# Kernel optimization log

Hardware: AMD Instinct MI355X
Metric: run time of the kernel (lower is better)

The kernel has to match this reference:

```python
import jax, jax.numpy as jnp
import numpy as np

HID = 512       # hidden_dim (embed/LSTM input)
HDE = 512       # hidden_dim_de == attn_channels (required by conv_att channel count)
NCLS = 7000
LSEQ = 40
B = 128
FH, FW = 8, 32


def setup_inputs() -> dict:
    key = jax.random.key(0)
    ks = jax.random.split(key, 16)
    s = 0.05
    inp = {
        "hidden_en": jax.random.normal(ks[0], (1, B, HID), jnp.float32),
        "x_em": jax.random.normal(ks[1], (B, HDE, FH, FW), jnp.float32),
        "att_x_em": jax.random.normal(ks[2], (B, FH * FW, HDE), jnp.float32),
        "target": jax.random.randint(ks[3], (B, LSEQ), 0, NCLS),
        "feature_h": FH,
        "feature_w": FW,
        # parameters
        "embed_w": jax.random.normal(ks[4], (NCLS, HID), jnp.float32) * s,
        "W_ih": jax.random.normal(ks[5], (4 * HDE, HID), jnp.float32) * s,   # LSTMCell input weights (i,f,g,o)
        "W_hh": jax.random.normal(ks[6], (4 * HDE, HDE), jnp.float32) * s,
        "b_ih": jax.random.normal(ks[7], (4 * HDE,), jnp.float32) * s,
        "b_hh": jax.random.normal(ks[8], (4 * HDE,), jnp.float32) * s,
        "hem_w": jax.random.normal(ks[9], (HDE, HDE), jnp.float32) * s,     # 1x1 conv h_em as matrix
        "hem_b": jax.random.normal(ks[10], (HDE,), jnp.float32) * s,
        "attw_w": jax.random.normal(ks[11], (HDE,), jnp.float32) * s,       # 1x1 conv conv_att -> 1 channel
        "attw_b": jax.random.normal(ks[12], (), jnp.float32) * s,
        "lin_w": jax.random.normal(ks[13], (NCLS, HDE + HDE), jnp.float32) * s,
        "lin_b": jax.random.normal(ks[14], (NCLS,), jnp.float32) * s,
    }
    return inp


def _decode(hidden_en, x_em, att_x_em, target, embed_w, W_ih, W_hh, b_ih, b_hh,
            hem_w, hem_b, attw_w, attw_b, lin_w, lin_b):
    L = target.shape[1]
    # teacher-forced inputs: step 0 uses hidden_en[-1], step t>=1 uses embed(target[:, t-1])
    xt0 = hidden_en[-1]                                   # [B, HID]
    xts = jnp.concatenate([xt0[None], jnp.transpose(embed_w[target[:, : L - 1]], (1, 0, 2))], axis=0)  # [L,B,HID]
    xg_all = jnp.einsum('lbi,gi->lbg', xts, W_ih) + b_ih  # precompute input gates [L,B,4H]
    Bn = x_em.shape[0]
    h0 = jnp.zeros((Bn, HDE), x_em.dtype)
    c0 = jnp.zeros((Bn, HDE), x_em.dtype)

    def step(carry, xg):
        h, c = carry
        gates = xg + h @ W_hh.T + b_hh
        i, f, g, o = jnp.split(gates, 4, axis=-1)
        c = jax.nn.sigmoid(f) * c + jax.nn.sigmoid(i) * jnp.tanh(g)
        h = jax.nn.sigmoid(o) * jnp.tanh(c)
        # additive attention (dropout treated as identity for determinism)
        hem = h @ hem_w.T + hem_b                          # [B, C]
        feat = jnp.tanh(x_em + hem[:, :, None, None])      # [B, C, H, W]
        feat_att = jnp.einsum('bchw,c->bhw', feat, attw_w) + attw_b
        alpha = jax.nn.softmax(feat_att.reshape(Bn, -1), axis=-1)  # [B, HW]
        att = jnp.einsum('bn,bnd->bd', alpha, att_x_em)    # [B, C]
        scores = jax.nn.log_softmax(jnp.concatenate([h, att], -1) @ lin_w.T + lin_b)
        return (h, c), scores

    _, ys = jax.lax.scan(step, (h0, c0), xg_all)           # ys: [L, B, NCLS]
    return jnp.transpose(ys, (1, 0, 2))                    # [B, L, NCLS]


def reference(hidden_en, x_em, att_x_em, target, feature_h, feature_w,
              embed_w, W_ih, W_hh, b_ih, b_hh, hem_w, hem_b, attw_w, attw_b,
              lin_w, lin_b):
    return _decode(hidden_en, x_em, att_x_em, target, embed_w, W_ih, W_hh,
                   b_ih, b_hh, hem_w, hem_b, attw_w, attw_b, lin_w, lin_b)
```

## Files before the change

kernel.cpp:

```cpp
#include <hip/hip_runtime.h>

#define B_    128
#define HIDD  512
#define NCLS  7000
#define NPAD  7040
#define LSEQ  40
#define MROWS 5120
#define TT    10

typedef __attribute__((ext_vector_type(8))) short bf16x8;
typedef __attribute__((ext_vector_type(4))) float f32x4;

__device__ __forceinline__ unsigned short f2bf(float x) {
  union { float f; unsigned u; } v; v.f = x;
  unsigned r = v.u + 0x7fffu + ((v.u >> 16) & 1u);
  return (unsigned short)(r >> 16);
}
__device__ __forceinline__ float bf2f(unsigned short h) {
  union { unsigned u; float f; } v; v.u = ((unsigned)h) << 16;
  return v.f;
}
__device__ __forceinline__ float sigm(float x) { return 1.f / (1.f + __expf(-x)); }
__device__ __forceinline__ float tanh_f(float x) {
  float e = __expf(2.f * x);
  return 1.f - 2.f / (e + 1.f);
}
__device__ __forceinline__ float rcp_f(float x) { return __builtin_amdgcn_rcpf(x); }

__global__ __launch_bounds__(256) void k_cvt(const float* __restrict__ src,
                                             unsigned short* __restrict__ dst, int n4) {
  int i = blockIdx.x * 256 + threadIdx.x;
  if (i >= n4) return;
  float4 v = ((const float4*)src)[i];
  ushort4 o; o.x = f2bf(v.x); o.y = f2bf(v.y); o.z = f2bf(v.z); o.w = f2bf(v.w);
  ((ushort4*)dst)[i] = o;
}

__global__ __launch_bounds__(256) void k_cvtp(const float* __restrict__ src,
                                              unsigned short* __restrict__ dst,
                                              const float* __restrict__ b1,
                                              const float* __restrict__ b2,
                                              float* __restrict__ bsum) {
  int i = blockIdx.x * 256 + threadIdx.x;
  int e = i * 4;
  int n = e >> 9, col = e & 511;
  int srow = ((n >> 4) & 3) * 512 + (n >> 6) * 16 + (n & 15);
  float4 v = *(const float4*)(src + (size_t)srow * 512 + col);
  ushort4 o; o.x = f2bf(v.x); o.y = f2bf(v.y); o.z = f2bf(v.z); o.w = f2bf(v.w);
  ((ushort4*)dst)[i] = o;
  if (bsum != nullptr && col == 0) bsum[n] = b1[srow] + b2[srow];
}

__global__ __launch_bounds__(256) void k_expcvt(const float* __restrict__ src,
                                                unsigned short* __restrict__ dst, int n4) {
  int i = blockIdx.x * 256 + threadIdx.x;
  if (i >= n4) return;
  float4 v = ((const float4*)src)[i];
  ushort4 o;
  o.x = f2bf(__expf(2.f * v.x)); o.y = f2bf(__expf(2.f * v.y));
  o.z = f2bf(__expf(2.f * v.z)); o.w = f2bf(__expf(2.f * v.w));
  ((ushort4*)dst)[i] = o;
}

__global__ __launch_bounds__(256) void k_linpad(const float* __restrict__ lw,
                                                unsigned short* __restrict__ dst) {
  int i = blockIdx.x * 256 + threadIdx.x;
  int e = i * 4;
  int row = e >> 10;
  ushort4 o;
  if (row < NCLS) {
    float4 v = *(const float4*)(lw + (size_t)row * 1024 + (e & 1023));
    o.x = f2bf(v.x); o.y = f2bf(v.y); o.z = f2bf(v.z); o.w = f2bf(v.w);
  } else { o.x = 0; o.y = 0; o.z = 0; o.w = 0; }
  ((ushort4*)dst)[i] = o;
}

__global__ __launch_bounds__(256) void k_xts(const float* __restrict__ hidden_en,
                                             const float* __restrict__ embed_w,
                                             const int* __restrict__ target,
                                             unsigned short* __restrict__ xts) {
  int i = blockIdx.x * 256 + threadIdx.x;
  int e = i * 4;
  int r = e >> 9, col = e & 511;
  int l = r >> 7, b = r & 127;
  const float* src;
  if (l == 0) src = hidden_en + b * 512 + col;
  else        src = embed_w + (size_t)target[b * LSEQ + (l - 1)] * 512 + col;
  float4 v = *(const float4*)src;
  ushort4 o; o.x = f2bf(v.x); o.y = f2bf(v.y); o.z = f2bf(v.z); o.w = f2bf(v.w);
  ((ushort4*)xts)[i] = o;
}

template <int MODE>
__global__ __launch_bounds__(256) void k_gemm(const unsigned short* __restrict__ A, int lda,
                                              const unsigned short* __restrict__ Bw, int ldb,
                                              const float* __restrict__ bias,
                                              void* __restrict__ outp, int ldc, int K) {
  __shared__ __align__(16) unsigned short As[128 * 32];
  __shared__ __align__(16) unsigned short Bs[128 * 32];
  const int tid = threadIdx.x;
  const int lane = tid & 63, wid = tid >> 6;
  const int wm = wid >> 1, wn = wid & 1;
  const int quad = lane >> 4, l16 = lane & 15;
  const int m0 = blockIdx.x * 128, n0 = blockIdx.y * 128;
  f32x4 acc[4][4];
#pragma unroll
  for (int i = 0; i < 4; i++)
#pragma unroll
    for (int j = 0; j < 4; j++) acc[i][j] = (f32x4){0.f, 0.f, 0.f, 0.f};

  const int r0 = tid >> 2, kq0 = (tid & 3) * 8;
  for (int k0 = 0; k0 < K; k0 += 32) {
#pragma unroll
    for (int s = 0; s < 2; s++) {
      int row = r0 + s * 64;
      *(bf16x8*)(As + row * 32 + kq0) = *(const bf16x8*)(A + (size_t)(m0 + row) * lda + k0 + kq0);
      *(bf16x8*)(Bs + row * 32 + kq0) = *(const bf16x8*)(Bw + (size_t)(n0 + row) * ldb + k0 + kq0);
    }
    __syncthreads();
    bf16x8 af[4], bfr[4];
#pragma unroll
    for (int i = 0; i < 4; i++)
      af[i] = *(const bf16x8*)(As + (wm * 64 + i * 16 + l16) * 32 + quad * 8);
#pragma unroll
    for (int j = 0; j < 4; j++)
      bfr[j] = *(const bf16x8*)(Bs + (wn * 64 + j * 16 + l16) * 32 + quad * 8);
#pragma unroll
    for (int i = 0; i < 4; i++)
#pragma unroll
      for (int j = 0; j < 4; j++)
        acc[i][j] = __builtin_amdgcn_mfma_f32_16x16x32_bf16(af[i], bfr[j], acc[i][j], 0, 0, 0);
    __syncthreads();
  }
#pragma unroll
  for (int i = 0; i < 4; i++) {
    int mbase = m0 + wm * 64 + i * 16 + quad * 4;
#pragma unroll
    for (int j = 0; j < 4; j++) {
      int n = n0 + wn * 64 + j * 16 + l16;
#pragma unroll
      for (int r = 0; r < 4; r++) {
        float v = acc[i][j][r];
        int m = mbase + r;
        if (MODE == 0) {
          ((unsigned short*)outp)[(size_t)m * ldc + n] = f2bf(v + bias[n]);
        } else if (MODE == 3) {
          ((float*)outp)[(size_t)m * ldc + n] = __expf(2.f * (v + bias[n]));
        } else {
          if (n < NCLS) {
            int t = m >> 7, b = m & 127;
            ((float*)outp)[((size_t)(b * LSEQ + t)) * NCLS + n] = v + bias[n];
          }
        }
      }
    }
  }
}

__global__ __launch_bounds__(256) void k_step(const unsigned short* __restrict__ h_prev,
                                              unsigned short* __restrict__ h_new,
                                              float* __restrict__ c_buf,
                                              const unsigned short* __restrict__ xg,
                                              const unsigned short* __restrict__ whhp,
                                              unsigned short* __restrict__ hatt, int t) {
  __shared__ __align__(16) unsigned short As[128 * 32];
  __shared__ __align__(16) unsigned short Bs[128 * 32];
  const int tid = threadIdx.x;
  const int lane = tid & 63, wid = tid >> 6;
  const int wm = wid >> 1, wn = wid & 1;
  const int quad = lane >> 4, l16 = lane & 15;
  const int n0 = blockIdx.x * 128;
  f32x4 acc[4][4];
#pragma unroll
  for (int i = 0; i < 4; i++)
#pragma unroll
    for (int j = 0; j < 4; j++) acc[i][j] = (f32x4){0.f, 0.f, 0.f, 0.f};

  if (t > 0) {
    const int r0 = tid >> 2, kq0 = (tid & 3) * 8;
    for (int k0 = 0; k0 < 512; k0 += 32) {
#pragma unroll
      for (int s = 0; s < 2; s++) {
        int row = r0 + s * 64;
        *(bf16x8*)(As + row * 32 + kq0) = *(const bf16x8*)(h_prev + (size_t)row * 512 + k0 + kq0);
        *(bf16x8*)(Bs + row * 32 + kq0) = *(const bf16x8*)(whhp + (size_t)(n0 + row) * 512 + k0 + kq0);
      }
      __syncthreads();
      bf16x8 af[4], bfr[4];
#pragma unroll
      for (int i = 0; i < 4; i++)
        af[i] = *(const bf16x8*)(As + (wm * 64 + i * 16 + l16) * 32 + quad * 8);
#pragma unroll
      for (int j = 0; j < 4; j++)
        bfr[j] = *(const bf16x8*)(Bs + (wn * 64 + j * 16 + l16) * 32 + quad * 8);
#pragma unroll
      for (int i = 0; i < 4; i++)
#pragma unroll
        for (int j = 0; j < 4; j++)
          acc[i][j] = __builtin_amdgcn_mfma_f32_16x16x32_bf16(af[i], bfr[j], acc[i][j], 0, 0, 0);
      __syncthreads();
    }
  }
  const int jcol = ((n0 >> 6) + wn) * 16 + l16;
#pragma unroll
  for (int i = 0; i < 4; i++) {
    int mbase = wm * 64 + i * 16 + quad * 4;
#pragma unroll
    for (int r = 0; r < 4; r++) {
      int m = mbase + r;
      const unsigned short* xrow = xg + (size_t)(t * 128 + m) * 2048 + n0 + wn * 64 + l16;
      float ip = acc[i][0][r] + bf2f(xrow[0]);
      float fp = acc[i][1][r] + bf2f(xrow[16]);
      float gp = acc[i][2][r] + bf2f(xrow[32]);
      float op = acc[i][3][r] + bf2f(xrow[48]);
      float c_old = (t > 0) ? c_buf[m * 512 + jcol] : 0.f;
      float c = sigm(fp) * c_old + sigm(ip) * tanh_f(gp);
      c_buf[m * 512 + jcol] = c;
      float h = sigm(op) * tanh_f(c);
      unsigned short hb = f2bf(h);
      h_new[m * 512 + jcol] = hb;
      hatt[(size_t)(t * 128 + m) * 1024 + jcol] = hb;
    }
  }
}

__global__ __launch_bounds__(256) void k_feat(const float* __restrict__ Eh,
                                              const unsigned short* __restrict__ Ex,
                                              const float* __restrict__ attw_w,
                                              float* __restrict__ s_all) {
  __shared__ float EhL[TT][512];
  __shared__ float wL[512];
  const int tid = threadIdx.x;
  const int tg = blockIdx.x >> 7, b = blockIdx.x & 127;
  const int t0 = tg * TT;
  for (int i = tid * 4; i < TT * 512; i += 1024) {
    int t = i >> 9, c = i & 511;
    *(float4*)&EhL[t][c] = *(const float4*)&Eh[((size_t)(t0 + t) * 128 + b) * 512 + c];
  }
  if (tid < 128) *(float4*)&wL[tid * 4] = *(const float4*)&attw_w[tid * 4];
  __syncthreads();
  const int p = tid;
  const unsigned short* xp = Ex + (size_t)b * 512 * 256 + p;
  float acc[TT];
#pragma unroll
  for (int t = 0; t < TT; t++) acc[t] = 0.f;
  for (int c0 = 0; c0 < 512; c0 += 4) {
    float ex0 = bf2f(xp[(size_t)(c0 + 0) * 256]);
    float ex1 = bf2f(xp[(size_t)(c0 + 1) * 256]);
    float ex2 = bf2f(xp[(size_t)(c0 + 2) * 256]);
    float ex3 = bf2f(xp[(size_t)(c0 + 3) * 256]);
    float4 wv = *(const float4*)&wL[c0];
#pragma unroll
    for (int t = 0; t < TT; t++) {
      float4 eh = *(const float4*)&EhL[t][c0];
      acc[t] = __builtin_fmaf(wv.x, rcp_f(__builtin_fmaf(ex0, eh.x, 1.f)), acc[t]);
      acc[t] = __builtin_fmaf(wv.y, rcp_f(__builtin_fmaf(ex1, eh.y, 1.f)), acc[t]);
      acc[t] = __builtin_fmaf(wv.z, rcp_f(__builtin_fmaf(ex2, eh.z, 1.f)), acc[t]);
      acc[t] = __builtin_fmaf(wv.w, rcp_f(__builtin_fmaf(ex3, eh.w, 1.f)), acc[t]);
    }
  }
#pragma unroll
  for (int t = 0; t < TT; t++)
    s_all[((size_t)(t0 + t) * 128 + b) * 256 + p] = -2.f * acc[t];
}

__global__ __launch_bounds__(256) void k_att(const float* __restrict__ s_all,
                                             const float* __restrict__ atx,
                                             unsigned short* __restrict__ hatt) {
  __shared__ float sL[40][257];
  __shared__ float zinv[40];
  const int tid = threadIdx.x;
  const int b = blockIdx.x >> 1, dh = blockIdx.x & 1;
  for (int i = tid; i < 40 * 256; i += 256) {
    int t = i >> 8, p = i & 255;
    sL[t][p] = s_all[((size_t)t * 128 + b) * 256 + p];
  }
  __syncthreads();
  if (tid < 40) {
    int t = tid;
    float mx = -1e30f;
    for (int p = 0; p < 256; p++) mx = fmaxf(mx, sL[t][p]);
    float z = 0.f;
    for (int p = 0; p < 256; p++) { float e = __expf(sL[t][p] - mx); sL[t][p] = e; z += e; }
    zinv[t] = 1.f / z;
  }
  __syncthreads();
  float acc[40];
#pragma unroll
  for (int t = 0; t < 40; t++) acc[t] = 0.f;
  const int d = dh * 256 + tid;
  const float* ap = atx + (size_t)b * 256 * 512 + d;
  for (int p = 0; p < 256; p++) {
    float av = ap[(size_t)p * 512];
#pragma unroll
    for (int t = 0; t < 40; t++) acc[t] += sL[t][p] * av;
  }
#pragma unroll
  for (int t = 0; t < 40; t++) {
    float v = acc[t] * zinv[t];
    hatt[((size_t)t * 128 + b) * 1024 + 512 + d] = f2bf(v);
  }
}

__global__ __launch_bounds__(256) void k_lsm(float* __restrict__ out) {
  __shared__ float buf[7000];
  __shared__ float red[256];
  const int tid = threadIdx.x;
  float* pr = out + (size_t)blockIdx.x * NCLS;
  for (int i = tid * 4; i < NCLS; i += 1024)
    *(float4*)&buf[i] = *(const float4*)&pr[i];
  __syncthreads();
  float mx = -1e30f;
  for (int i = tid; i < NCLS; i += 256) mx = fmaxf(mx, buf[i]);
  red[tid] = mx; __syncthreads();
  for (int s = 128; s > 0; s >>= 1) { if (tid < s) red[tid] = fmaxf(red[tid], red[tid + s]); __syncthreads(); }
  mx = red[0]; __syncthreads();
  float sum = 0.f;
  for (int i = tid; i < NCLS; i += 256) sum += __expf(buf[i] - mx);
  red[tid] = sum; __syncthreads();
  for (int s = 128; s > 0; s >>= 1) { if (tid < s) red[tid] += red[tid + s]; __syncthreads(); }
  float lse = mx + __logf(red[0]);
  for (int i = tid * 4; i < NCLS; i += 1024) {
    float4 v = *(const float4*)&buf[i];
    v.x -= lse; v.y -= lse; v.z -= lse; v.w -= lse;
    *(float4*)&pr[i] = v;
  }
}

extern "C" void kernel_launch(void* const* d_in, const int* in_sizes, int n_in,
                              void* d_out, int out_size, void* d_ws, size_t ws_size,
                              hipStream_t stream) {
  const float* hidden_en = (const float*)d_in[0];
  const float* x_em      = (const float*)d_in[1];
  const float* att_x     = (const float*)d_in[2];
  const int*   target    = (const int*)d_in[3];
  const float* embed_w   = (const float*)d_in[6];
  const float* W_ih      = (const float*)d_in[7];
  const float* W_hh      = (const float*)d_in[8];
  const float* b_ih      = (const float*)d_in[9];
  const float* b_hh      = (const float*)d_in[10];
  const float* hem_w     = (const float*)d_in[11];
  const float* hem_b     = (const float*)d_in[12];
  const float* attw_w    = (const float*)d_in[13];
  const float* lin_w     = (const float*)d_in[15];
  const float* lin_b     = (const float*)d_in[16];
  float* out = (float*)d_out;
  (void)in_sizes; (void)n_in; (void)out_size; (void)ws_size;

  char* w = (char*)d_ws;
  size_t off = 0;
  auto alloc = [&](size_t bytes) { char* p = w + off; off = (off + bytes + 255) & ~(size_t)255; return p; };
  unsigned short* xts  = (unsigned short*)alloc((size_t)MROWS * 512 * 2);
  unsigned short* wihp = (unsigned short*)alloc((size_t)2048 * 512 * 2);
  unsigned short* whhp = (unsigned short*)alloc((size_t)2048 * 512 * 2);
  unsigned short* xg   = (unsigned short*)alloc((size_t)MROWS * 2048 * 2);
  unsigned short* hemw = (unsigned short*)alloc((size_t)512 * 512 * 2);
  unsigned short* linw = (unsigned short*)alloc((size_t)NPAD * 1024 * 2);
  unsigned short* xem  = (unsigned short*)alloc((size_t)128 * 512 * 256 * 2);
  unsigned short* hatt = (unsigned short*)alloc((size_t)MROWS * 1024 * 2);
  unsigned short* h0   = (unsigned short*)alloc((size_t)128 * 512 * 2);
  unsigned short* h1   = (unsigned short*)alloc((size_t)128 * 512 * 2);
  float* cb      = (float*)alloc((size_t)128 * 512 * 4);
  float* bsum    = (float*)alloc((size_t)2048 * 4);
  float* eh_all  = (float*)alloc((size_t)MROWS * 512 * 4);
  float* s_all   = (float*)alloc((size_t)MROWS * 256 * 4);

  k_cvtp<<<1024, 256, 0, stream>>>(W_ih, wihp, b_ih, b_hh, bsum);
  k_cvtp<<<1024, 256, 0, stream>>>(W_hh, whhp, nullptr, nullptr, nullptr);
  k_cvt<<<256, 256, 0, stream>>>(hem_w, hemw, 512 * 512 / 4);
  k_expcvt<<<16384, 256, 0, stream>>>(x_em, xem, 128 * 512 * 256 / 4);
  k_linpad<<<NPAD * 1024 / 4 / 256, 256, 0, stream>>>(lin_w, linw);
  k_xts<<<MROWS * 512 / 4 / 256, 256, 0, stream>>>(hidden_en, embed_w, target, xts);
  k_gemm<0><<<dim3(40, 16), 256, 0, stream>>>(xts, 512, wihp, 512, bsum, xg, 2048, 512);

  for (int t = 0; t < LSEQ; t++) {
    const unsigned short* hp = (t & 1) ? h0 : h1;
    unsigned short* hn = (t & 1) ? h1 : h0;
    k_step<<<16, 256, 0, stream>>>(hp, hn, cb, xg, whhp, hatt, t);
  }

  k_gemm<3><<<dim3(40, 4), 256, 0, stream>>>(hatt, 1024, hemw, 512, hem_b, eh_all, 512, 512);
  k_feat<<<512, 256, 0, stream>>>(eh_all, xem, attw_w, s_all);
  k_att<<<256, 256, 0, stream>>>(s_all, att_x, hatt);

  k_gemm<2><<<dim3(40, 55), 256, 0, stream>>>(hatt, 1024, linw, 1024, lin_b, out, NCLS, 1024);
  k_lsm<<<MROWS, 256, 0, stream>>>(out);
}
```

Measured before the change: 1.317 ms.

## Fuse LSTM recurrence into persistent cooperative kernel and use direct-to-LDS GEMM loads

Replaces the 40 per-timestep k_step launches with one cooperative persistent kernel of 16 blocks. Each block keeps its slice of W_hh resident in swizzled LDS and its cell state in registers, and the blocks meet at a global atomic-counter barrier after every step. This removes the per-step launch cost and the repeated W_hh reloads, at the price of spin-wait barrier latency. Separately, the shared GEMM's tile loads now use global_load_lds to copy straight into LDS instead of going through registers.

After: 1.408 ms. 1.07x slower.

```diff
diff --git a/kernel.cpp b/kernel.cpp
--- a/kernel.cpp
+++ b/kernel.cpp
@@ -7,6 +7,7 @@
 #define LSEQ  40
 #define MROWS 5120
 #define TT    10
+#define SBLK  16
 
 typedef __attribute__((ext_vector_type(8))) short bf16x8;
 typedef __attribute__((ext_vector_type(4))) float f32x4;
@@ -26,6 +27,14 @@
   return 1.f - 2.f / (e + 1.f);
 }
 __device__ __forceinline__ float rcp_f(float x) { return __builtin_amdgcn_rcpf(x); }
+
+__device__ __forceinline__ void gl_lds16(const void* g, void* l) {
+  auto gp = reinterpret_cast<const __attribute__((address_space(1))) unsigned int*>(
+      reinterpret_cast<unsigned long long>(g));
+  auto lp = reinterpret_cast<__attribute__((address_space(3))) unsigned int*>(
+      reinterpret_cast<unsigned long long>(l));
+  __builtin_amdgcn_global_load_lds(gp, lp, 16, 0, 0);
+}
 
 __global__ __launch_bounds__(256) void k_cvt(const float* __restrict__ src,
                                              unsigned short* __restrict__ dst, int n4) {
@@ -78,7 +87,10 @@
 __global__ __launch_bounds__(256) void k_xts(const float* __restrict__ hidden_en,
                                              const float* __restrict__ embed_w,
                                              const int* __restrict__ target,
-                                             unsigned short* __restrict__ xts) {
+                                             unsigned short* __restrict__ xts,
+                                             int* __restrict__ cnt) {
+  if (blockIdx.x == 0 && threadIdx.x == 0)
+    __hip_atomic_store(cnt, 0, __ATOMIC_RELAXED, __HIP_MEMORY_SCOPE_AGENT);
   int i = blockIdx.x * 256 + threadIdx.x;
   int e = i * 4;
   int r = e >> 9, col = e & 511;
@@ -102,6 +114,7 @@
   const int lane = tid & 63, wid = tid >> 6;
   const int wm = wid >> 1, wn = wid & 1;
   const int quad = lane >> 4, l16 = lane & 15;
+  const int gr = lane >> 2, gc = (lane & 3) * 8;
   const int m0 = blockIdx.x * 128, n0 = blockIdx.y * 128;
   f32x4 acc[4][4];
 #pragma unroll
@@ -109,13 +122,12 @@
 #pragma unroll
     for (int j = 0; j < 4; j++) acc[i][j] = (f32x4){0.f, 0.f, 0.f, 0.f};
 
-  const int r0 = tid >> 2, kq0 = (tid & 3) * 8;
   for (int k0 = 0; k0 < K; k0 += 32) {
 #pragma unroll
     for (int s = 0; s < 2; s++) {
-      int row = r0 + s * 64;
-      *(bf16x8*)(As + row * 32 + kq0) = *(const bf16x8*)(A + (size_t)(m0 + row) * lda + k0 + kq0);
-      *(bf16x8*)(Bs + row * 32 + kq0) = *(const bf16x8*)(Bw + (size_t)(n0 + row) * ldb + k0 + kq0);
+      const int rb = s * 64 + wid * 16;
+      gl_lds16(A + (size_t)(m0 + rb + gr) * lda + k0 + gc, As + rb * 32);
+      gl_lds16(Bw + (size_t)(n0 + rb + gr) * ldb + k0 + gc, Bs + rb * 32);
     }
     __syncthreads();
     bf16x8 af[4], bfr[4];
@@ -220,6 +232,95 @@
       unsigned short hb = f2bf(h);
       h_new[m * 512 + jcol] = hb;
       hatt[(size_t)(t * 128 + m) * 1024 + jcol] = hb;
+    }
+  }
+}
+
+__global__ __launch_bounds__(256) void k_scan3(unsigned short* __restrict__ h0,
+                                               unsigned short* __restrict__ h1,
+                                               const unsigned short* __restrict__ xg,
+                                               const unsigned short* __restrict__ whhp,
+                                               unsigned short* __restrict__ hatt,
+                                               int* __restrict__ cnt) {
+  __shared__ __align__(16) unsigned short Wl[128 * 512];
+  const int tid = threadIdx.x;
+  const int lane = tid & 63, wid = tid >> 6;
+  const int wm = wid >> 1, wn = wid & 1;
+  const int quad = lane >> 4, l16 = lane & 15;
+  const int n0 = blockIdx.x * 128;
+
+  for (int i = tid; i < 128 * 64; i += 256) {
+    int row = i >> 6, c8 = (i & 63) << 3;
+    bf16x8 v = *(const bf16x8*)(whhp + (size_t)(n0 + row) * 512 + c8);
+    *(bf16x8*)((char*)Wl + ((row * 1024 + c8 * 2) ^ ((row & 7) << 4))) = v;
+  }
+  float cst[4][4];
+#pragma unroll
+  for (int i = 0; i < 4; i++)
+#pragma unroll
+    for (int r = 0; r < 4; r++) cst[i][r] = 0.f;
+  const int jcol = ((n0 >> 6) + wn) * 16 + l16;
+  __syncthreads();
+
+  for (int t = 0; t < LSEQ; t++) {
+    f32x4 acc[4][4];
+#pragma unroll
+    for (int i = 0; i < 4; i++)
+#pragma unroll
+      for (int j = 0; j < 4; j++) acc[i][j] = (f32x4){0.f, 0.f, 0.f, 0.f};
+    if (t > 0) {
+      const unsigned short* hp = (t & 1) ? h0 : h1;
+      const unsigned short* hb = hp + (size_t)(wm * 64 + l16) * 512 + quad * 8;
+#pragma unroll 4
+      for (int k0 = 0; k0 < 512; k0 += 32) {
+        bf16x8 af[4], bfr[4];
+#pragma unroll
+        for (int i = 0; i < 4; i++)
+          af[i] = *(const bf16x8*)(hb + (size_t)i * 16 * 512 + k0);
+#pragma unroll
+        for (int j = 0; j < 4; j++) {
+          int rw = wn * 64 + j * 16 + l16;
+          bfr[j] = *(const bf16x8*)((const char*)Wl +
+                    ((rw * 1024 + (k0 + quad * 8) * 2) ^ ((rw & 7) << 4)));
+        }
+#pragma unroll
+        for (int i = 0; i < 4; i++)
+#pragma unroll
+          for (int j = 0; j < 4; j++)
+            acc[i][j] = __builtin_amdgcn_mfma_f32_16x16x32_bf16(af[i], bfr[j], acc[i][j], 0, 0, 0);
+      }
+    }
+    unsigned short* hn = (t & 1) ? h1 : h0;
+    const unsigned short* xq = xg + (size_t)(t * 128) * 2048 + n0 + wn * 64 + l16;
+#pragma unroll
+    for (int i = 0; i < 4; i++) {
+#pragma unroll
+      for (int r = 0; r < 4; r++) {
+        int m = wm * 64 + i * 16 + quad * 4 + r;
+        const unsigned short* xrow = xq + (size_t)m * 2048;
+        float ip = acc[i][0][r] + bf2f(xrow[0]);
+        float fp = acc[i][1][r] + bf2f(xrow[16]);
+        float gp = acc[i][2][r] + bf2f(xrow[32]);
+        float op = acc[i][3][r] + bf2f(xrow[48]);
+        float c = sigm(fp) * cst[i][r] + sigm(ip) * tanh_f(gp);
+        cst[i][r] = c;
+        float h = sigm(op) * tanh_f(c);
+        unsigned short hbv = f2bf(h);
+        hn[m * 512 + jcol] = hbv;
+        hatt[(size_t)(t * 128 + m) * 1024 + jcol] = hbv;
+      }
+    }
+    if (t < LSEQ - 1) {
+      __threadfence();
+      __syncthreads();
+      if (tid == 0) {
+        __hip_atomic_fetch_add(cnt, 1, __ATOMIC_RELEASE, __HIP_MEMORY_SCOPE_AGENT);
+        const int tgt = SBLK * (t + 1);
+        while (__hip_atomic_load(cnt, __ATOMIC_ACQUIRE, __HIP_MEMORY_SCOPE_AGENT) < tgt)
+          __builtin_amdgcn_s_sleep(8);
+      }
+      __syncthreads();
+      __threadfence();
     }
   }
 }
@@ -364,19 +465,26 @@
   float* bsum    = (float*)alloc((size_t)2048 * 4);
   float* eh_all  = (float*)alloc((size_t)MROWS * 512 * 4);
   float* s_all   = (float*)alloc((size_t)MROWS * 256 * 4);
+  int*   cnt     = (int*)alloc(256);
 
   k_cvtp<<<1024, 256, 0, stream>>>(W_ih, wihp, b_ih, b_hh, bsum);
   k_cvtp<<<1024, 256, 0, stream>>>(W_hh, whhp, nullptr, nullptr, nullptr);
   k_cvt<<<256, 256, 0, stream>>>(hem_w, hemw, 512 * 512 / 4);
   k_expcvt<<<16384, 256, 0, stream>>>(x_em, xem, 128 * 512 * 256 / 4);
   k_linpad<<<NPAD * 1024 / 4 / 256, 256, 0, stream>>>(lin_w, linw);
-  k_xts<<<MROWS * 512 / 4 / 256, 256, 0, stream>>>(hidden_en, embed_w, target, xts);
+  k_xts<<<MROWS * 512 / 4 / 256, 256, 0, stream>>>(hidden_en, embed_w, target, xts, cnt);
   k_gemm<0><<<dim3(40, 16), 256, 0, stream>>>(xts, 512, wihp, 512, bsum, xg, 2048, 512);
 
-  for (int t = 0; t < LSEQ; t++) {
-    const unsigned short* hp = (t & 1) ? h0 : h1;
-    unsigned short* hn = (t & 1) ? h1 : h0;
-    k_step<<<16, 256, 0, stream>>>(hp, hn, cb, xg, whhp, hatt, t);
+  {
+    void* args[] = { (void*)&h0, (void*)&h1, (void*)&xg, (void*)&whhp, (void*)&hatt, (void*)&cnt };
+    hipError_t ce = hipLaunchCooperativeKernel(k_scan3, dim3(SBLK), dim3(256), args, 0u, stream);
+    if (ce != hipSuccess) {
+      for (int t = 0; t < LSEQ; t++) {
+        const unsigned short* hp = (t & 1) ? h0 : h1;
+        unsigned short* hn = (t & 1) ? h1 : h0;
+        k_step<<<16, 256, 0, stream>>>(hp, hn, cb, xg, whhp, hatt, t);
+      }
+    }
   }
 
   k_gemm<3><<<dim3(40, 4), 256, 0, stream>>>(hatt, 1024, hemw, 512, hem_b, eh_all, 512, 512);
```
